# Optimization experiments

Measured on AMD Instinct MI355X. Metric: run time of the kernel, lower is better.

Reference implementation:

```python
import jax, jax.numpy as jnp
import numpy as np

B, S, D, H, E = 4, 1024, 1024, 2048, 8
TOP_K = 2


def setup_inputs() -> dict:
    key = jax.random.key(0)
    ks = jax.random.split(key, 8)
    s = 0.02
    return {
        "x": jax.random.normal(ks[0], (B, S, D), dtype=jnp.float32),
        "tgt_pad": jnp.zeros((B, S), dtype=bool),
        "W1": jax.random.normal(ks[1], (E, H, D), dtype=jnp.float32) * s,
        "W2": jax.random.normal(ks[2], (E, D, H), dtype=jnp.float32) * s,
        "W3": jax.random.normal(ks[3], (E, H, D), dtype=jnp.float32) * s,
        "Wg": jax.random.normal(ks[4], (E, D), dtype=jnp.float32) * s,
        "Wc": jax.random.normal(ks[5], (1, D), dtype=jnp.float32) * s,
        "bc": jnp.zeros((1,), dtype=jnp.float32),
    }


def reference(x, tgt_pad, W1, W2, W3, Wg, Wc, bc):
    b, s, d = x.shape
    xf = x.reshape(-1, d)  # [N, D], N = B*S

    # token gating (temperature = 1.0)
    gate_logits = xf @ Wg.T  # [N, E]
    routing = jax.nn.softmax(gate_logits.astype(jnp.float32), axis=1)
    routing_full = routing.reshape(b, s, E)  # returned as routing_weights_

    # top-k selection and renormalization
    rw, sel = jax.lax.top_k(routing, TOP_K)  # [N, K]
    rw = rw / rw.sum(axis=-1, keepdims=True)
    rw = rw.astype(x.dtype)

    # per-token per-expert combine weight (0 if expert not in top-k)
    onehot = jax.nn.one_hot(sel, E, dtype=x.dtype)  # [N, K, E]
    combined = jnp.einsum('nk,nke->ne', rw, onehot)  # [N, E]

    # dense-equivalent expert loop: unselected tokens get weight 0,
    # identical math to torch gather/index_add since weight multiplies output
    final = jnp.zeros_like(xf)
    cls_logits = []
    for e in range(E):
        h = jax.nn.silu(xf @ W1[e].T) * (xf @ W3[e].T)  # [N, H]
        contrib = (h @ W2[e].T) * combined[:, e, None]  # [N, D]
        final = final + contrib
        # classifier on CLS token of the running accumulation (cumulative)
        cls = final.reshape(b, s, d)[:, 0, :]  # [B, D]
        cls_logits.append(cls @ Wc.T + bc)  # [B, 1]
    expert_logits = jnp.stack(cls_logits)  # [E, B, 1]

    return final.reshape(b, s, d), gate_logits, expert_logits, routing_full
```

## Files before the change

### kernel.cpp

```cpp
#include <hip/hip_runtime.h>

#define NTOK 4096
#define DDIM 1024
#define HDIM 2048
#define NEXP 8
#define SEQ  1024

typedef float f32x4 __attribute__((ext_vector_type(4)));
typedef __bf16 bf16x8 __attribute__((ext_vector_type(8)));
typedef unsigned short u16x8 __attribute__((ext_vector_type(8)));

__device__ __forceinline__ unsigned short f2bf(float f) {
  unsigned int u = __float_as_uint(f);
  u += 0x7fffu + ((u >> 16) & 1u);
  return (unsigned short)(u >> 16);
}

__device__ __forceinline__ u16x8 pack8(const float4& a, const float4& b) {
  u16x8 r;
  r[0] = f2bf(a.x); r[1] = f2bf(a.y); r[2] = f2bf(a.z); r[3] = f2bf(a.w);
  r[4] = f2bf(b.x); r[5] = f2bf(b.y); r[6] = f2bf(b.z); r[7] = f2bf(b.w);
  return r;
}

__device__ __forceinline__ void gl_lds16(const unsigned short* g, unsigned short* l) {
  __builtin_amdgcn_global_load_lds(
      (__attribute__((address_space(1))) unsigned int*)g,
      (__attribute__((address_space(3))) unsigned int*)l, 16, 0, 0);
}

__global__ __launch_bounds__(256) void f2bf_kernel(
    const float* __restrict__ src, unsigned short* __restrict__ dst, int n8) {
  for (int i = blockIdx.x * 256 + threadIdx.x; i < n8; i += gridDim.x * 256) {
    const float4* s = (const float4*)src + (size_t)i * 2;
    float4 a = s[0], b = s[1];
    ((u16x8*)dst)[i] = pack8(a, b);
  }
}

__global__ __launch_bounds__(256) void moe_gating(
    const float* __restrict__ x, const float* __restrict__ Wg,
    float* __restrict__ out_gate, float* __restrict__ out_rout,
    int* __restrict__ counts, int* __restrict__ idxlist,
    float* __restrict__ wlist, unsigned short* __restrict__ xb) {
  const int wave = threadIdx.x >> 6;
  const int lane = threadIdx.x & 63;
  const int n = blockIdx.x * 4 + wave;

  const float4* xp = (const float4*)(x + (size_t)n * DDIM + lane * 16);
  float4 xv0 = xp[0], xv1 = xp[1], xv2 = xp[2], xv3 = xp[3];

  u16x8* xrow = (u16x8*)(xb + ((size_t)n << 10));
  xrow[lane * 2]     = pack8(xv0, xv1);
  xrow[lane * 2 + 1] = pack8(xv2, xv3);

  float acc[NEXP];
#pragma unroll
  for (int e = 0; e < NEXP; ++e) {
    const float4* wp = (const float4*)(Wg + e * DDIM + lane * 16);
    float4 w0 = wp[0], w1 = wp[1], w2 = wp[2], w3 = wp[3];
    float a = xv0.x * w0.x + xv0.y * w0.y + xv0.z * w0.z + xv0.w * w0.w;
    a += xv1.x * w1.x + xv1.y * w1.y + xv1.z * w1.z + xv1.w * w1.w;
    a += xv2.x * w2.x + xv2.y * w2.y + xv2.z * w2.z + xv2.w * w2.w;
    a += xv3.x * w3.x + xv3.y * w3.y + xv3.z * w3.z + xv3.w * w3.w;
    acc[e] = a;
  }
#pragma unroll
  for (int e = 0; e < NEXP; ++e)
    for (int off = 32; off; off >>= 1) acc[e] += __shfl_xor(acc[e], off);

  float mx = acc[0];
#pragma unroll
  for (int e = 1; e < NEXP; ++e) mx = fmaxf(mx, acc[e]);
  float ex[NEXP], s = 0.f;
#pragma unroll
  for (int e = 0; e < NEXP; ++e) { ex[e] = __expf(acc[e] - mx); s += ex[e]; }
  const float inv = 1.f / s;

  if (lane < NEXP) {
    out_gate[n * NEXP + lane] = acc[lane];
    out_rout[n * NEXP + lane] = ex[lane] * inv;
  }

  if (lane == 0) {
    int e0 = 0; float l0 = acc[0];
#pragma unroll
    for (int e = 1; e < NEXP; ++e) if (acc[e] > l0) { l0 = acc[e]; e0 = e; }
    int e1 = -1; float l1 = -1e30f;
#pragma unroll
    for (int e = 0; e < NEXP; ++e)
      if (e != e0 && acc[e] > l1) { l1 = acc[e]; e1 = e; }
    const float p0 = ex[e0], p1 = ex[e1];
    const float rinv = 1.f / (p0 + p1);
    int pos0 = atomicAdd(&counts[e0], 1);
    idxlist[e0 * NTOK + pos0] = n * 2;     wlist[e0 * NTOK + pos0] = p0 * rinv;
    int pos1 = atomicAdd(&counts[e1], 1);
    idxlist[e1 * NTOK + pos1] = n * 2 + 1; wlist[e1 * NTOK + pos1] = p1 * rinv;
  }
}

__global__ __launch_bounds__(256) void moe_gemm1(
    const unsigned short* __restrict__ xb, const unsigned short* __restrict__ W1b,
    const unsigned short* __restrict__ W3b, const int* __restrict__ counts,
    const int* __restrict__ idxlist, unsigned short* __restrict__ h_ws) {
  const int e = blockIdx.z;
  const int count = counts[e];
  const int m0 = blockIdx.y * 128;
  if (m0 >= count) return;
  const int n0 = blockIdx.x * 64;

  __shared__ unsigned short As[128 * 64];
  __shared__ unsigned short B1s[64 * 64];
  __shared__ unsigned short B3s[64 * 64];
  __shared__ int s_entry[128];

  const int tid = threadIdx.x;
  const int lane = tid & 63;
  const int wave = tid >> 6;
  if (tid < 128) {
    int r = m0 + tid;
    s_entry[tid] = (r < count) ? idxlist[e * NTOK + r] : 0;
  }
  __syncthreads();

  const int cswz = ((lane & 7) ^ (lane >> 3)) << 3;

  const unsigned short* gA[4]; unsigned short* lA[4];
#pragma unroll
  for (int t = 0; t < 4; ++t) {
    const int rb = (wave << 5) + (t << 3);
    const int r = rb + (lane >> 3);
    gA[t] = xb + ((size_t)(s_entry[r] >> 1) << 10) + cswz;
    lA[t] = &As[rb << 6];
  }
  const unsigned short* w1p = W1b + ((size_t)e << 21);
  const unsigned short* w3p = W3b + ((size_t)e << 21);
  const unsigned short* gB1[2]; const unsigned short* gB3[2];
  unsigned short* lB1[2]; unsigned short* lB3[2];
#pragma unroll
  for (int t = 0; t < 2; ++t) {
    const int rb = (wave << 4) + (t << 3);
    const int r = rb + (lane >> 3);
    gB1[t] = w1p + ((size_t)(n0 + r) << 10) + cswz;
    gB3[t] = w3p + ((size_t)(n0 + r) << 10) + cswz;
    lB1[t] = &B1s[rb << 6];
    lB3[t] = &B3s[rb << 6];
  }

  const int wm = wave >> 1, wn = wave & 1;
  const int l16 = lane & 15, quad = lane >> 4;
  const int lsw = l16 & 7;

  f32x4 acc1[4][2], acc3[4][2];
  const f32x4 zero = {0.f, 0.f, 0.f, 0.f};
#pragma unroll
  for (int i = 0; i < 4; ++i)
#pragma unroll
    for (int j = 0; j < 2; ++j) { acc1[i][j] = zero; acc3[i][j] = zero; }

  for (int k0 = 0; k0 < DDIM; k0 += 64) {
#pragma unroll
    for (int t = 0; t < 4; ++t) gl_lds16(gA[t] + k0, lA[t]);
#pragma unroll
    for (int t = 0; t < 2; ++t) {
      gl_lds16(gB1[t] + k0, lB1[t]);
      gl_lds16(gB3[t] + k0, lB3[t]);
    }
    __syncthreads();
#pragma unroll
    for (int ks = 0; ks < 2; ++ks) {
      const int co = (((ks << 2) + quad) ^ lsw) << 3;
      bf16x8 a[4], b1[2], b3[2];
#pragma unroll
      for (int i = 0; i < 4; ++i) {
        const int row = (wm << 6) + (i << 4) + l16;
        a[i] = *(const bf16x8*)&As[(row << 6) + co];
      }
#pragma unroll
      for (int j = 0; j < 2; ++j) {
        const int row = (wn << 5) + (j << 4) + l16;
        b1[j] = *(const bf16x8*)&B1s[(row << 6) + co];
        b3[j] = *(const bf16x8*)&B3s[(row << 6) + co];
      }
#pragma unroll
      for (int i = 0; i < 4; ++i)
#pragma unroll
        for (int j = 0; j < 2; ++j) {
          acc1[i][j] = __builtin_amdgcn_mfma_f32_16x16x32_bf16(a[i], b1[j], acc1[i][j], 0, 0, 0);
          acc3[i][j] = __builtin_amdgcn_mfma_f32_16x16x32_bf16(a[i], b3[j], acc3[i][j], 0, 0, 0);
        }
    }
    __syncthreads();
  }
#pragma unroll
  for (int i = 0; i < 4; ++i) {
#pragma unroll
    for (int reg = 0; reg < 4; ++reg) {
      const int rl = (wm << 6) + (i << 4) + (quad << 2) + reg;
      if (m0 + rl < count) {
        const int entry = s_entry[rl];
#pragma unroll
        for (int j = 0; j < 2; ++j) {
          const float c1 = acc1[i][j][reg];
          const float c3 = acc3[i][j][reg];
          const float hv = (c1 / (1.f + __expf(-c1))) * c3;
          const int col = n0 + (wn << 5) + (j << 4) + l16;
          h_ws[(size_t)entry * HDIM + col] = f2bf(hv);
        }
      }
    }
  }
}

__global__ __launch_bounds__(256) void moe_gemm2(
    const unsigned short* __restrict__ h_ws, const unsigned short* __restrict__ W2b,
    const int* __restrict__ counts, const int* __restrict__ idxlist,
    const float* __restrict__ wlist, float* __restrict__ contrib,
    float* __restrict__ clsbuf) {
  const int e = blockIdx.z;
  const int count = counts[e];
  const int m0 = blockIdx.y * 128;
  if (m0 >= count) return;
  const int n0 = blockIdx.x * 128;

  __shared__ unsigned short As[128 * 64];
  __shared__ unsigned short Bs[128 * 64];
  __shared__ int s_entry[128];
  __shared__ float s_w[128];

  const int tid = threadIdx.x;
  const int lane = tid & 63;
  const int wave = tid >> 6;
  if (tid < 128) {
    int r = m0 + tid;
    s_entry[tid] = (r < count) ? idxlist[e * NTOK + r] : 0;
    s_w[tid] = (r < count) ? wlist[e * NTOK + r] : 0.f;
  }
  __syncthreads();

  const int cswz = ((lane & 7) ^ (lane >> 3)) << 3;

  const unsigned short* gA[4]; unsigned short* lA[4];
  const unsigned short* gB[4]; unsigned short* lB[4];
  const unsigned short* w2p = W2b + ((size_t)e << 21);
#pragma unroll
  for (int t = 0; t < 4; ++t) {
    const int rb = (wave << 5) + (t << 3);
    const int r = rb + (lane >> 3);
    gA[t] = h_ws + ((size_t)s_entry[r] << 11) + cswz;
    lA[t] = &As[rb << 6];
    gB[t] = w2p + ((size_t)(n0 + r) << 11) + cswz;
    lB[t] = &Bs[rb << 6];
  }

  const int wm = wave >> 1, wn = wave & 1;
  const int l16 = lane & 15, quad = lane >> 4;
  const int lsw = l16 & 7;

  f32x4 acc[4][4];
  const f32x4 zero = {0.f, 0.f, 0.f, 0.f};
#pragma unroll
  for (int i = 0; i < 4; ++i)
#pragma unroll
    for (int j = 0; j < 4; ++j) acc[i][j] = zero;

  for (int k0 = 0; k0 < HDIM; k0 += 64) {
#pragma unroll
    for (int t = 0; t < 4; ++t) {
      gl_lds16(gA[t] + k0, lA[t]);
      gl_lds16(gB[t] + k0, lB[t]);
    }
    __syncthreads();
#pragma unroll
    for (int ks = 0; ks < 2; ++ks) {
      const int co = (((ks << 2) + quad) ^ lsw) << 3;
      bf16x8 a[4], b[4];
#pragma unroll
      for (int i = 0; i < 4; ++i) {
        const int row = (wm << 6) + (i << 4) + l16;
        a[i] = *(const bf16x8*)&As[(row << 6) + co];
      }
#pragma unroll
      for (int j = 0; j < 4; ++j) {
        const int row = (wn << 6) + (j << 4) + l16;
        b[j] = *(const bf16x8*)&Bs[(row << 6) + co];
      }
#pragma unroll
      for (int i = 0; i < 4; ++i)
#pragma unroll
        for (int j = 0; j < 4; ++j)
          acc[i][j] = __builtin_amdgcn_mfma_f32_16x16x32_bf16(a[i], b[j], acc[i][j], 0, 0, 0);
    }
    __syncthreads();
  }
#pragma unroll
  for (int i = 0; i < 4; ++i) {
#pragma unroll
    for (int reg = 0; reg < 4; ++reg) {
      const int rl = (wm << 6) + (i << 4) + (quad << 2) + reg;
      if (m0 + rl < count) {
        const int entry = s_entry[rl];
        const int tok = entry >> 1;
        const float w = s_w[rl];
        const bool is_cls = (tok & (SEQ - 1)) == 0;
#pragma unroll
        for (int j = 0; j < 4; ++j) {
          const int col = n0 + (wn << 6) + (j << 4) + l16;
          const float v = acc[i][j][reg] * w;
          contrib[((size_t)entry << 10) + col] = v;
          if (is_cls) clsbuf[(e * 4 + (tok >> 10)) * DDIM + col] = v;
        }
      }
    }
  }
}

__global__ __launch_bounds__(256) void moe_combine(
    const float* __restrict__ contrib, float* __restrict__ out_final) {
  const int i = blockIdx.x * 256 + threadIdx.x;
  const int tok = i >> 8, c4 = i & 255;
  const float4* cp = (const float4*)contrib;
  float4 a = cp[((size_t)tok * 2) * 256 + c4];
  float4 b = cp[((size_t)tok * 2 + 1) * 256 + c4];
  float4 o; o.x = a.x + b.x; o.y = a.y + b.y; o.z = a.z + b.z; o.w = a.w + b.w;
  ((float4*)out_final)[i] = o;
}

__global__ __launch_bounds__(256) void moe_elog(
    const float* __restrict__ clsbuf, const float* __restrict__ Wc,
    const float* __restrict__ bcp, float* __restrict__ out_elog) {
  __shared__ float t[32];
  const int wave = threadIdx.x >> 6;
  const int lane = threadIdx.x & 63;
  for (int p = wave; p < 32; p += 4) {
    const float4* vp = (const float4*)(clsbuf + (size_t)p * DDIM + lane * 16);
    const float4* wp = (const float4*)(Wc + lane * 16);
    float a = 0.f;
#pragma unroll
    for (int q = 0; q < 4; ++q) {
      float4 v = vp[q], w = wp[q];
      a += v.x * w.x + v.y * w.y + v.z * w.z + v.w * w.w;
    }
    for (int off = 32; off; off >>= 1) a += __shfl_xor(a, off);
    if (lane == 0) t[p] = a;
  }
  __syncthreads();
  if (threadIdx.x < 4) {
    const int b = threadIdx.x;
    float run = 0.f;
    const float bias = bcp[0];
#pragma unroll
    for (int e = 0; e < NEXP; ++e) {
      run += t[e * 4 + b];
      out_elog[e * 4 + b] = run + bias;
    }
  }
}

extern "C" void kernel_launch(void* const* d_in, const int* in_sizes, int n_in,
                              void* d_out, int out_size, void* d_ws, size_t ws_size,
                              hipStream_t stream) {
  const float* x  = (const float*)d_in[0];
  const float* W1 = (const float*)d_in[2];
  const float* W2 = (const float*)d_in[3];
  const float* W3 = (const float*)d_in[4];
  const float* Wg = (const float*)d_in[5];
  const float* Wc = (const float*)d_in[6];
  const float* bc = (const float*)d_in[7];

  float* out_final = (float*)d_out;
  float* out_gate  = out_final + 4194304;
  float* out_elog  = out_gate + 32768;
  float* out_rout  = out_elog + 32;

  char* ws = (char*)d_ws;
  int*   counts  = (int*)ws;
  int*   idxlist = (int*)(ws + 1024);
  float* wlist   = (float*)(ws + 132096);
  float* clsbuf  = (float*)(ws + 263168);
  const size_t MB = 1u << 20;
  unsigned short* h_ws = (unsigned short*)(ws + MB);
  unsigned short* xb   = (unsigned short*)(ws + 33 * MB);
  unsigned short* W1b  = (unsigned short*)(ws + 41 * MB);
  unsigned short* W3b  = (unsigned short*)(ws + 73 * MB);
  unsigned short* W2b  = W1b;
  float* contrib = (float*)(ws + 73 * MB);

  hipMemsetAsync(ws, 0, 1024, stream);
  hipMemsetAsync((void*)clsbuf, 0, 131072, stream);

  f2bf_kernel<<<4096, 256, 0, stream>>>(W1, W1b, 2097152);
  f2bf_kernel<<<4096, 256, 0, stream>>>(W3, W3b, 2097152);
  moe_gating<<<1024, 256, 0, stream>>>(x, Wg, out_gate, out_rout,
                                       counts, idxlist, wlist, xb);
  moe_gemm1<<<dim3(32, 32, 8), 256, 0, stream>>>(xb, W1b, W3b, counts, idxlist, h_ws);
  f2bf_kernel<<<4096, 256, 0, stream>>>(W2, W2b, 2097152);
  moe_gemm2<<<dim3(8, 32, 8), 256, 0, stream>>>(h_ws, W2b, counts, idxlist, wlist,
                                                contrib, clsbuf);
  moe_combine<<<4096, 256, 0, stream>>>(contrib, out_final);
  moe_elog<<<1, 256, 0, stream>>>(clsbuf, Wc, bc, out_elog);
}
```

Baseline: 507.8 us.

## Fuse prep and final kernels, shrink gemm2 M-tile, drop LDS index staging

The gating kernel and the W1/W3 bf16 conversions are merged into one launch with extra blocks doing the conversion, and the combine and expert-logit kernels are merged into one launch. The two memsets become one by moving clsbuf next to counts. gemm2's M-tile goes from 128 to 64 rows, doubling grid.y, and both GEMMs gain an occupancy hint (launch_bounds 256,5). The shared-memory index/weight staging and its barrier are replaced by direct global reads of idxlist/wlist. The aim is fewer launches, less tail waste on uneven expert counts and higher occupancy. In exchange there are more redundant global index loads and less B-tile reuse in gemm2.

Result: slower. 859.2 us (+69.2%).

```diff
diff --git a/kernel.cpp b/kernel.cpp
--- a/kernel.cpp
+++ b/kernel.cpp
@@ -29,20 +29,26 @@
       (__attribute__((address_space(3))) unsigned int*)l, 16, 0, 0);
 }
 
-__global__ __launch_bounds__(256) void f2bf_kernel(
-    const float* __restrict__ src, unsigned short* __restrict__ dst, int n8) {
-  for (int i = blockIdx.x * 256 + threadIdx.x; i < n8; i += gridDim.x * 256) {
-    const float4* s = (const float4*)src + (size_t)i * 2;
-    float4 a = s[0], b = s[1];
-    ((u16x8*)dst)[i] = pack8(a, b);
-  }
-}
-
-__global__ __launch_bounds__(256) void moe_gating(
+__global__ __launch_bounds__(256) void moe_prep(
     const float* __restrict__ x, const float* __restrict__ Wg,
+    const float* __restrict__ W1, const float* __restrict__ W3,
     float* __restrict__ out_gate, float* __restrict__ out_rout,
     int* __restrict__ counts, int* __restrict__ idxlist,
-    float* __restrict__ wlist, unsigned short* __restrict__ xb) {
+    float* __restrict__ wlist, unsigned short* __restrict__ xb,
+    unsigned short* __restrict__ W1b, unsigned short* __restrict__ W3b) {
+  if (blockIdx.x >= 1024) {
+    const int base = (blockIdx.x - 1024) * 256 + threadIdx.x;
+    for (int g = base; g < 4194304; g += 2048 * 256) {
+      const int half = g >> 21;
+      const int off = g & 2097151;
+      const float* src = half ? W3 : W1;
+      unsigned short* dst = half ? W3b : W1b;
+      const float4* s = (const float4*)src + (size_t)off * 2;
+      float4 a = s[0], b = s[1];
+      ((u16x8*)dst)[off] = pack8(a, b);
+    }
+    return;
+  }
   const int wave = threadIdx.x >> 6;
   const int lane = threadIdx.x & 63;
   const int n = blockIdx.x * 4 + wave;
@@ -99,7 +105,16 @@
   }
 }
 
-__global__ __launch_bounds__(256) void moe_gemm1(
+__global__ __launch_bounds__(256) void f2bf_kernel(
+    const float* __restrict__ src, unsigned short* __restrict__ dst, int n8) {
+  for (int i = blockIdx.x * 256 + threadIdx.x; i < n8; i += gridDim.x * 256) {
+    const float4* s = (const float4*)src + (size_t)i * 2;
+    float4 a = s[0], b = s[1];
+    ((u16x8*)dst)[i] = pack8(a, b);
+  }
+}
+
+__global__ __launch_bounds__(256, 5) void moe_gemm1(
     const unsigned short* __restrict__ xb, const unsigned short* __restrict__ W1b,
     const unsigned short* __restrict__ W3b, const int* __restrict__ counts,
     const int* __restrict__ idxlist, unsigned short* __restrict__ h_ws) {
@@ -112,16 +127,11 @@
   __shared__ unsigned short As[128 * 64];
   __shared__ unsigned short B1s[64 * 64];
   __shared__ unsigned short B3s[64 * 64];
-  __shared__ int s_entry[128];
 
   const int tid = threadIdx.x;
   const int lane = tid & 63;
   const int wave = tid >> 6;
-  if (tid < 128) {
-    int r = m0 + tid;
-    s_entry[tid] = (r < count) ? idxlist[e * NTOK + r] : 0;
-  }
-  __syncthreads();
+  const int* ilp = idxlist + e * NTOK;
 
   const int cswz = ((lane & 7) ^ (lane >> 3)) << 3;
 
@@ -130,7 +140,8 @@
   for (int t = 0; t < 4; ++t) {
     const int rb = (wave << 5) + (t << 3);
     const int r = rb + (lane >> 3);
-    gA[t] = xb + ((size_t)(s_entry[r] >> 1) << 10) + cswz;
+    const int entry = (m0 + r < count) ? ilp[m0 + r] : 0;
+    gA[t] = xb + ((size_t)(entry >> 1) << 10) + cswz;
     lA[t] = &As[rb << 6];
   }
   const unsigned short* w1p = W1b + ((size_t)e << 21);
@@ -198,7 +209,7 @@
     for (int reg = 0; reg < 4; ++reg) {
       const int rl = (wm << 6) + (i << 4) + (quad << 2) + reg;
       if (m0 + rl < count) {
-        const int entry = s_entry[rl];
+        const int entry = ilp[m0 + rl];
 #pragma unroll
         for (int j = 0; j < 2; ++j) {
           const float c1 = acc1[i][j][reg];
@@ -212,43 +223,42 @@
   }
 }
 
-__global__ __launch_bounds__(256) void moe_gemm2(
+__global__ __launch_bounds__(256, 5) void moe_gemm2(
     const unsigned short* __restrict__ h_ws, const unsigned short* __restrict__ W2b,
     const int* __restrict__ counts, const int* __restrict__ idxlist,
     const float* __restrict__ wlist, float* __restrict__ contrib,
     float* __restrict__ clsbuf) {
   const int e = blockIdx.z;
   const int count = counts[e];
-  const int m0 = blockIdx.y * 128;
+  const int m0 = blockIdx.y * 64;
   if (m0 >= count) return;
   const int n0 = blockIdx.x * 128;
 
-  __shared__ unsigned short As[128 * 64];
+  __shared__ unsigned short As[64 * 64];
   __shared__ unsigned short Bs[128 * 64];
-  __shared__ int s_entry[128];
-  __shared__ float s_w[128];
 
   const int tid = threadIdx.x;
   const int lane = tid & 63;
   const int wave = tid >> 6;
-  if (tid < 128) {
-    int r = m0 + tid;
-    s_entry[tid] = (r < count) ? idxlist[e * NTOK + r] : 0;
-    s_w[tid] = (r < count) ? wlist[e * NTOK + r] : 0.f;
-  }
-  __syncthreads();
+  const int* ilp = idxlist + e * NTOK;
 
   const int cswz = ((lane & 7) ^ (lane >> 3)) << 3;
 
-  const unsigned short* gA[4]; unsigned short* lA[4];
+  const unsigned short* gA[2]; unsigned short* lA[2];
+#pragma unroll
+  for (int t = 0; t < 2; ++t) {
+    const int rb = (wave << 4) + (t << 3);
+    const int r = rb + (lane >> 3);
+    const int entry = (m0 + r < count) ? ilp[m0 + r] : 0;
+    gA[t] = h_ws + ((size_t)entry << 11) + cswz;
+    lA[t] = &As[rb << 6];
+  }
+  const unsigned short* w2p = W2b + ((size_t)e << 21);
   const unsigned short* gB[4]; unsigned short* lB[4];
-  const unsigned short* w2p = W2b + ((size_t)e << 21);
 #pragma unroll
   for (int t = 0; t < 4; ++t) {
     const int rb = (wave << 5) + (t << 3);
     const int r = rb + (lane >> 3);
-    gA[t] = h_ws + ((size_t)s_entry[r] << 11) + cswz;
-    lA[t] = &As[rb << 6];
     gB[t] = w2p + ((size_t)(n0 + r) << 11) + cswz;
     lB[t] = &Bs[rb << 6];
   }
@@ -257,27 +267,26 @@
   const int l16 = lane & 15, quad = lane >> 4;
   const int lsw = l16 & 7;
 
-  f32x4 acc[4][4];
+  f32x4 acc[2][4];
   const f32x4 zero = {0.f, 0.f, 0.f, 0.f};
 #pragma unroll
-  for (int i = 0; i < 4; ++i)
+  for (int i = 0; i < 2; ++i)
 #pragma unroll
     for (int j = 0; j < 4; ++j) acc[i][j] = zero;
 
   for (int k0 = 0; k0 < HDIM; k0 += 64) {
 #pragma unroll
-    for (int t = 0; t < 4; ++t) {
-      gl_lds16(gA[t] + k0, lA[t]);
-      gl_lds16(gB[t] + k0, lB[t]);
-    }
+    for (int t = 0; t < 2; ++t) gl_lds16(gA[t] + k0, lA[t]);
+#pragma unroll
+    for (int t = 0; t < 4; ++t) gl_lds16(gB[t] + k0, lB[t]);
     __syncthreads();
 #pragma unroll
     for (int ks = 0; ks < 2; ++ks) {
       const int co = (((ks << 2) + quad) ^ lsw) << 3;
-      bf16x8 a[4], b[4];
-#pragma unroll
-      for (int i = 0; i < 4; ++i) {
-        const int row = (wm << 6) + (i << 4) + l16;
+      bf16x8 a[2], b[4];
+#pragma unroll
+      for (int i = 0; i < 2; ++i) {
+        const int row = (wm << 5) + (i << 4) + l16;
         a[i] = *(const bf16x8*)&As[(row << 6) + co];
       }
 #pragma unroll
@@ -286,7 +295,7 @@
         b[j] = *(const bf16x8*)&Bs[(row << 6) + co];
       }
 #pragma unroll
-      for (int i = 0; i < 4; ++i)
+      for (int i = 0; i < 2; ++i)
 #pragma unroll
         for (int j = 0; j < 4; ++j)
           acc[i][j] = __builtin_amdgcn_mfma_f32_16x16x32_bf16(a[i], b[j], acc[i][j], 0, 0, 0);
@@ -294,14 +303,14 @@
     __syncthreads();
   }
 #pragma unroll
-  for (int i = 0; i < 4; ++i) {
+  for (int i = 0; i < 2; ++i) {
 #pragma unroll
     for (int reg = 0; reg < 4; ++reg) {
-      const int rl = (wm << 6) + (i << 4) + (quad << 2) + reg;
+      const int rl = (wm << 5) + (i << 4) + (quad << 2) + reg;
       if (m0 + rl < count) {
-        const int entry = s_entry[rl];
+        const int entry = ilp[m0 + rl];
+        const float w = wlist[e * NTOK + m0 + rl];
         const int tok = entry >> 1;
-        const float w = s_w[rl];
         const bool is_cls = (tok & (SEQ - 1)) == 0;
 #pragma unroll
         for (int j = 0; j < 4; ++j) {
@@ -315,8 +324,39 @@
   }
 }
 
-__global__ __launch_bounds__(256) void moe_combine(
-    const float* __restrict__ contrib, float* __restrict__ out_final) {
+__global__ __launch_bounds__(256) void moe_final(
+    const float* __restrict__ contrib, float* __restrict__ out_final,
+    const float* __restrict__ clsbuf, const float* __restrict__ Wc,
+    const float* __restrict__ bcp, float* __restrict__ out_elog) {
+  if (blockIdx.x == 4096) {
+    __shared__ float t[32];
+    const int wave = threadIdx.x >> 6;
+    const int lane = threadIdx.x & 63;
+    for (int p = wave; p < 32; p += 4) {
+      const float4* vp = (const float4*)(clsbuf + (size_t)p * DDIM + lane * 16);
+      const float4* wp = (const float4*)(Wc + lane * 16);
+      float a = 0.f;
+#pragma unroll
+      for (int q = 0; q < 4; ++q) {
+        float4 v = vp[q], w = wp[q];
+        a += v.x * w.x + v.y * w.y + v.z * w.z + v.w * w.w;
+      }
+      for (int off = 32; off; off >>= 1) a += __shfl_xor(a, off);
+      if (lane == 0) t[p] = a;
+    }
+    __syncthreads();
+    if (threadIdx.x < 4) {
+      const int b = threadIdx.x;
+      float run = 0.f;
+      const float bias = bcp[0];
+#pragma unroll
+      for (int e = 0; e < NEXP; ++e) {
+        run += t[e * 4 + b];
+        out_elog[e * 4 + b] = run + bias;
+      }
+    }
+    return;
+  }
   const int i = blockIdx.x * 256 + threadIdx.x;
   const int tok = i >> 8, c4 = i & 255;
   const float4* cp = (const float4*)contrib;
@@ -324,37 +364,6 @@
   float4 b = cp[((size_t)tok * 2 + 1) * 256 + c4];
   float4 o; o.x = a.x + b.x; o.y = a.y + b.y; o.z = a.z + b.z; o.w = a.w + b.w;
   ((float4*)out_final)[i] = o;
-}
-
-__global__ __launch_bounds__(256) void moe_elog(
-    const float* __restrict__ clsbuf, const float* __restrict__ Wc,
-    const float* __restrict__ bcp, float* __restrict__ out_elog) {
-  __shared__ float t[32];
-  const int wave = threadIdx.x >> 6;
-  const int lane = threadIdx.x & 63;
-  for (int p = wave; p < 32; p += 4) {
-    const float4* vp = (const float4*)(clsbuf + (size_t)p * DDIM + lane * 16);
-    const float4* wp = (const float4*)(Wc + lane * 16);
-    float a = 0.f;
-#pragma unroll
-    for (int q = 0; q < 4; ++q) {
-      float4 v = vp[q], w = wp[q];
-      a += v.x * w.x + v.y * w.y + v.z * w.z + v.w * w.w;
-    }
-    for (int off = 32; off; off >>= 1) a += __shfl_xor(a, off);
-    if (lane == 0) t[p] = a;
-  }
-  __syncthreads();
-  if (threadIdx.x < 4) {
-    const int b = threadIdx.x;
-    float run = 0.f;
-    const float bias = bcp[0];
-#pragma unroll
-    for (int e = 0; e < NEXP; ++e) {
-      run += t[e * 4 + b];
-      out_elog[e * 4 + b] = run + bias;
-    }
-  }
 }
 
 extern "C" void kernel_launch(void* const* d_in, const int* in_sizes, int n_in,
@@ -375,9 +384,9 @@
 
   char* ws = (char*)d_ws;
   int*   counts  = (int*)ws;
-  int*   idxlist = (int*)(ws + 1024);
-  float* wlist   = (float*)(ws + 132096);
-  float* clsbuf  = (float*)(ws + 263168);
+  float* clsbuf  = (float*)(ws + 1024);
+  int*   idxlist = (int*)(ws + 132096);
+  float* wlist   = (float*)(ws + 263168);
   const size_t MB = 1u << 20;
   unsigned short* h_ws = (unsigned short*)(ws + MB);
   unsigned short* xb   = (unsigned short*)(ws + 33 * MB);
@@ -386,17 +395,13 @@
   unsigned short* W2b  = W1b;
   float* contrib = (float*)(ws + 73 * MB);
 
-  hipMemsetAsync(ws, 0, 1024, stream);
-  hipMemsetAsync((void*)clsbuf, 0, 131072, stream);
-
-  f2bf_kernel<<<4096, 256, 0, stream>>>(W1, W1b, 2097152);
-  f2bf_kernel<<<4096, 256, 0, stream>>>(W3, W3b, 2097152);
-  moe_gating<<<1024, 256, 0, stream>>>(x, Wg, out_gate, out_rout,
-                                       counts, idxlist, wlist, xb);
+  hipMemsetAsync(ws, 0, 132096, stream);
+
+  moe_prep<<<3072, 256, 0, stream>>>(x, Wg, W1, W3, out_gate, out_rout,
+                                     counts, idxlist, wlist, xb, W1b, W3b);
   moe_gemm1<<<dim3(32, 32, 8), 256, 0, stream>>>(xb, W1b, W3b, counts, idxlist, h_ws);
   f2bf_kernel<<<4096, 256, 0, stream>>>(W2, W2b, 2097152);
-  moe_gemm2<<<dim3(8, 32, 8), 256, 0, stream>>>(h_ws, W2b, counts, idxlist, wlist,
+  moe_gemm2<<<dim3(8, 64, 8), 256, 0, stream>>>(h_ws, W2b, counts, idxlist, wlist,
                                                 contrib, clsbuf);
-  moe_combine<<<4096, 256, 0, stream>>>(contrib, out_final);
-  moe_elog<<<1, 256, 0, stream>>>(clsbuf, Wc, bc, out_elog);
-}
+  moe_final<<<4097, 256, 0, stream>>>(contrib, out_final, clsbuf, Wc, bc, out_elog);
+}
```
